# Kernel tuning notes

Measured on AMD Instinct MI355X. Metric: run time of the kernel, lower is better.

## Reference

```python
import jax, jax.numpy as jnp
import numpy as np

E = 8       # num_experts
K = 2       # top_k
N = 16384   # tokens
H = 2048    # hidden_dim
B = 128     # bottleneck_dim
EPS = 1e-6


def setup_inputs() -> dict:
    key = jax.random.key(0)
    ks = jax.random.split(key, 8)
    x = jax.random.normal(ks[0], (N, H), dtype=jnp.float32)
    skin_probs = jax.random.uniform(ks[1], (N, 3), dtype=jnp.float32)
    # routers (torch Linear weight layout: [out, in])
    W_img = jax.random.normal(ks[2], (E, H), dtype=jnp.float32) * 0.02
    W_skin = jax.random.normal(ks[3], (E, 3), dtype=jnp.float32) * 0.02
    # stacked expert params: Linear(H->B) then Linear(B->H)
    W1 = jax.random.normal(ks[4], (E, B, H), dtype=jnp.float32) * 0.02
    b1 = jax.random.normal(ks[5], (E, B), dtype=jnp.float32) * 0.02
    W2 = jax.random.normal(ks[6], (E, H, B), dtype=jnp.float32) * 0.02
    b2 = jax.random.normal(ks[7], (E, H), dtype=jnp.float32) * 0.02
    return {"x": x, "skin_probs": skin_probs, "W_img": W_img, "W_skin": W_skin,
            "W1": W1, "b1": b1, "W2": W2, "b2": b2}


def reference(x, skin_probs, W_img, W_skin, W1, b1, W2, b2):
    # router
    router_logits = x @ W_img.T + skin_probs @ W_skin.T          # [N, E]
    router_probs = jax.nn.softmax(router_logits, axis=-1)        # [N, E]
    top_v, top_i = jax.lax.top_k(router_probs, K)                 # [N, K]
    top_v = top_v / (top_v.sum(axis=-1, keepdims=True) + EPS)
    sel = jax.nn.one_hot(top_i, E, dtype=x.dtype)                 # [N, K, E], 0/1
    w = (sel * top_v[..., None]).sum(axis=1)                      # [N, E] combine weights (0 if not selected)
    # experts, dense-equivalent combine: out = sum_e w[n,e] * (relu(x W1_e^T + b1_e) W2_e^T + b2_e)
    h = jax.nn.relu(jnp.einsum('nh,ebh->neb', x, W1) + b1)        # [N, E, B]
    moe = jnp.einsum('neb,ehb->nh', h * w[:, :, None], W2) + w @ b2  # [N, H]
    out = x + moe
    # aux load-balancing loss
    mean_prob = router_probs.mean(axis=0)                         # [E]
    mean_freq = sel.sum(axis=1).mean(axis=0)                      # [E]
    aux_loss = (mean_prob * mean_freq).sum() * E
    return out, aux_loss
```

## Files before the change

### kernel.cpp

```cpp
#include <hip/hip_runtime.h>

#define N_TOK 16384
#define HD    2048
#define BD    128
#define NE    8
#define KEXT  1088

typedef float  f32x4  __attribute__((ext_vector_type(4)));
typedef __bf16 bf16x8 __attribute__((ext_vector_type(8)));
typedef unsigned short u16;
typedef unsigned short u16x4 __attribute__((ext_vector_type(4)));

__device__ __forceinline__ u16 f2bf(float f) {
  union { float f; unsigned u; } v; v.f = f;
  unsigned u = v.u;
  return (u16)((u + 0x7FFFu + ((u >> 16) & 1u)) >> 16);
}

__device__ __forceinline__ void gload16(const void* g, void* l) {
  __builtin_amdgcn_global_load_lds(
      (const __attribute__((address_space(1))) void*)g,
      (__attribute__((address_space(3))) void*)l, 16, 0, 0);
}

__global__ void init_aux_k(float* p) {
  if (threadIdx.x < 16) p[threadIdx.x] = 0.f;
}

__global__ __launch_bounds__(256) void conv_w1_k(const float* __restrict__ W1,
                                                 u16* __restrict__ W1b) {
  int i = (blockIdx.x * 256 + threadIdx.x) * 4;
  float4 v = *(const float4*)(W1 + i);
  u16x4 o; o.x = f2bf(v.x); o.y = f2bf(v.y); o.z = f2bf(v.z); o.w = f2bf(v.w);
  *(u16x4*)(W1b + i) = o;
}

__global__ __launch_bounds__(256) void conv_w2_k(const float* __restrict__ W2,
                                                 const float* __restrict__ b2,
                                                 u16* __restrict__ Bt2) {
  int i4 = (blockIdx.x * 256 + threadIdx.x) * 4;
  int h = i4 / KEXT, j0 = i4 % KEXT;
  u16x4 o;
  #pragma unroll
  for (int c = 0; c < 4; c++) {
    int j = j0 + c;
    float v;
    if (j < 1024) {
      int e = j >> 7, b = j & 127;
      v = W2[((size_t)e * HD + h) * BD + b];
    } else if (j < 1032) {
      v = b2[(size_t)(j - 1024) * HD + h];
    } else {
      v = 0.f;
    }
    if (c == 0) o.x = f2bf(v); else if (c == 1) o.y = f2bf(v);
    else if (c == 2) o.z = f2bf(v); else o.w = f2bf(v);
  }
  *(u16x4*)(Bt2 + i4) = o;
}

__global__ __launch_bounds__(256)
void router_k(const float* __restrict__ x, const float* __restrict__ skin,
              const float* __restrict__ Wimg, const float* __restrict__ Wskin,
              u16* __restrict__ xbf, float* __restrict__ wout,
              u16* __restrict__ h2, float* __restrict__ psum,
              float* __restrict__ cnt) {
  __shared__ float red[16];
  int t = threadIdx.x;
  int l = t & 63, wv = t >> 6;
  float pacc = 0.f, cacc = 0.f;

  for (int it = 0; it < 4; it++) {
    int n = blockIdx.x * 16 + wv * 4 + it;
    const float4* xr = (const float4*)(x + (size_t)n * HD);
    u16* xo = xbf + (size_t)n * HD;
    float4 xv[8];
    #pragma unroll
    for (int j = 0; j < 8; j++) {
      xv[j] = xr[j * 64 + l];
      u16x4 o; o.x = f2bf(xv[j].x); o.y = f2bf(xv[j].y);
      o.z = f2bf(xv[j].z); o.w = f2bf(xv[j].w);
      *(u16x4*)(xo + j * 256 + l * 4) = o;
    }
    float acc[NE];
    #pragma unroll
    for (int e = 0; e < NE; e++) {
      const float4* wr = (const float4*)(Wimg + (size_t)e * HD);
      float a = 0.f;
      #pragma unroll
      for (int j = 0; j < 8; j++) {
        float4 w4 = wr[j * 64 + l];
        a += xv[j].x * w4.x + xv[j].y * w4.y + xv[j].z * w4.z + xv[j].w * w4.w;
      }
      acc[e] = a;
    }
    float logit[NE];
    #pragma unroll
    for (int e = 0; e < NE; e++) {
      float v = acc[e];
      for (int off = 32; off >= 1; off >>= 1) v += __shfl_xor(v, off);
      logit[e] = v + skin[n * 3 + 0] * Wskin[e * 3 + 0]
                   + skin[n * 3 + 1] * Wskin[e * 3 + 1]
                   + skin[n * 3 + 2] * Wskin[e * 3 + 2];
    }
    float mx = logit[0];
    #pragma unroll
    for (int e = 1; e < NE; e++) mx = fmaxf(mx, logit[e]);
    float p[NE], s = 0.f;
    #pragma unroll
    for (int e = 0; e < NE; e++) { p[e] = expf(logit[e] - mx); s += p[e]; }
    float inv = 1.f / s;
    #pragma unroll
    for (int e = 0; e < NE; e++) p[e] *= inv;
    int i1 = 0; float v1 = p[0];
    #pragma unroll
    for (int e = 1; e < NE; e++) if (p[e] > v1) { v1 = p[e]; i1 = e; }
    int i2 = -1; float v2 = -1.f;
    #pragma unroll
    for (int e = 0; e < NE; e++) if (e != i1 && p[e] > v2) { v2 = p[e]; i2 = e; }
    float denom = v1 + v2 + 1e-6f;
    float w1v = v1 / denom, w2v = v2 / denom;
    float wl = (l == i1) ? w1v : ((l == i2) ? w2v : 0.f);
    if (l < NE) wout[(size_t)n * NE + l] = wl;
    h2[(size_t)n * KEXT + 1024 + l] = (l < NE) ? f2bf(wl) : (u16)0;
    if (l < NE) { pacc += p[l]; cacc += (l == i1 ? 1.f : 0.f) + (l == i2 ? 1.f : 0.f); }
  }
  __syncthreads();
  if (t < 16) red[t] = 0.f;
  __syncthreads();
  if (l < NE) { atomicAdd(&red[l], pacc); atomicAdd(&red[NE + l], cacc); }
  __syncthreads();
  if (t < 8)       atomicAdd(&psum[t], red[t]);
  else if (t < 16) atomicAdd(&cnt[t - 8], red[t]);
}

template <int EPI>
__global__ __launch_bounds__(256)
void gemm_bt(const u16* __restrict__ A, int lda,
             const u16* __restrict__ Bt, int ldb,
             int K, int NB, int chunk,
             const float* __restrict__ b1, const float* __restrict__ w,
             u16* __restrict__ Hout,
             const float* __restrict__ xres, float* __restrict__ out) {
  __shared__ u16 lA[128 * 64];
  __shared__ u16 lB[128 * 64];
  int xcd = blockIdx.x & 7, idxw = blockIdx.x >> 3;
  int lin = xcd * chunk + idxw;
  int bn = lin % NB, bm = lin / NB;

  int t = threadIdx.x;
  int l = t & 63, wv = t >> 6;
  int wr = wv >> 1, wc = wv & 1;
  int r = t >> 3;
  int cl = (t & 7) * 8;
  int cs = (((t & 7) ^ (r & 7))) * 8;

  const u16* Ag = A + (size_t)(bm * 128 + r) * lda + cs;
  const u16* Bg = Bt + (size_t)(bn * 128 + r) * ldb + cs;
  u16* lAp = &lA[r * 64 + cl];
  u16* lBp = &lB[r * 64 + cl];

  int swz = (l & 7) << 4;

  f32x4 acc[4][4];
  #pragma unroll
  for (int m = 0; m < 4; m++)
    #pragma unroll
    for (int n = 0; n < 4; n++) acc[m][n] = (f32x4){0.f, 0.f, 0.f, 0.f};

  for (int k0 = 0; k0 < K; k0 += 64) {
    #pragma unroll
    for (int i = 0; i < 4; i++) {
      gload16(Ag + (size_t)i * 32 * lda + k0, lAp + i * 32 * 64);
      gload16(Bg + (size_t)i * 32 * ldb + k0, lBp + i * 32 * 64);
    }
    __syncthreads();
    #pragma unroll
    for (int kk = 0; kk < 64; kk += 32) {
      int cb = (kk + (l >> 4) * 8) * 2;
      int co = cb ^ swz;
      bf16x8 a[4], b[4];
      #pragma unroll
      for (int m = 0; m < 4; m++) {
        int Ra = wr * 64 + m * 16 + (l & 15);
        a[m] = *(const bf16x8*)((const char*)lA + Ra * 128 + co);
      }
      #pragma unroll
      for (int n = 0; n < 4; n++) {
        int Rb = wc * 64 + n * 16 + (l & 15);
        b[n] = *(const bf16x8*)((const char*)lB + Rb * 128 + co);
      }
      #pragma unroll
      for (int m = 0; m < 4; m++)
        #pragma unroll
        for (int n = 0; n < 4; n++)
          acc[m][n] = __builtin_amdgcn_mfma_f32_16x16x32_bf16(a[m], b[n], acc[m][n], 0, 0, 0);
    }
    __syncthreads();
  }

  int row0 = bm * 128 + wr * 64 + (l >> 4) * 4;
  int col0 = bn * 128 + wc * 64 + (l & 15);
  if (EPI == 1) {
    #pragma unroll
    for (int n = 0; n < 4; n++) {
      int col = col0 + n * 16;
      float b1v = b1[col];
      #pragma unroll
      for (int m = 0; m < 4; m++) {
        #pragma unroll
        for (int j = 0; j < 4; j++) {
          int row = row0 + m * 16 + j;
          float v = acc[m][n][j] + b1v;
          v = v > 0.f ? v : 0.f;
          v *= w[(size_t)row * NE + bn];
          Hout[(size_t)row * KEXT + col] = f2bf(v);
        }
      }
    }
  } else {
    #pragma unroll
    for (int m = 0; m < 4; m++) {
      #pragma unroll
      for (int j = 0; j < 4; j++) {
        int row = row0 + m * 16 + j;
        const float* xr = xres + (size_t)row * HD;
        float* orow = out + (size_t)row * HD;
        #pragma unroll
        for (int n = 0; n < 4; n++) {
          int col = col0 + n * 16;
          orow[col] = acc[m][n][j] + xr[col];
        }
      }
    }
  }
}

__global__ void aux_fin_k(const float* __restrict__ psum,
                          const float* __restrict__ cnt,
                          float* __restrict__ out) {
  if (threadIdx.x == 0) {
    float a = 0.f;
    for (int e = 0; e < NE; e++)
      a += (psum[e] / (float)N_TOK) * (cnt[e] / (float)N_TOK);
    out[(size_t)N_TOK * HD] = a * (float)NE;
  }
}

extern "C" void kernel_launch(void* const* d_in, const int* in_sizes, int n_in,
                              void* d_out, int out_size, void* d_ws, size_t ws_size,
                              hipStream_t stream) {
  const float* x     = (const float*)d_in[0];
  const float* skin  = (const float*)d_in[1];
  const float* Wimg  = (const float*)d_in[2];
  const float* Wskin = (const float*)d_in[3];
  const float* W1    = (const float*)d_in[4];
  const float* b1    = (const float*)d_in[5];
  const float* W2    = (const float*)d_in[6];
  const float* b2    = (const float*)d_in[7];
  float* out = (float*)d_out;

  char* ws = (char*)d_ws;
  u16*   xbf  = (u16*)(ws);
  float* wout = (float*)(ws + 67108864);
  u16*   h2   = (u16*)(ws + 67633152);
  u16*   W1b  = (u16*)(ws + 103284736);
  u16*   Bt2  = (u16*)(ws + 107479040);
  float* aux  = (float*)(ws + 111935488);
  float* psum = aux;
  float* cnt  = aux + 8;

  init_aux_k<<<1, 64, 0, stream>>>(aux);
  conv_w1_k<<<(NE * BD * HD) / (256 * 4), 256, 0, stream>>>(W1, W1b);
  conv_w2_k<<<(HD * KEXT) / (256 * 4), 256, 0, stream>>>(W2, b2, Bt2);
  router_k<<<N_TOK / 16, 256, 0, stream>>>(x, skin, Wimg, Wskin, xbf, wout, h2,
                                           psum, cnt);
  aux_fin_k<<<1, 64, 0, stream>>>(psum, cnt, out);
  gemm_bt<1><<<(N_TOK / 128) * (1024 / 128), 256, 0, stream>>>(
      xbf, HD, W1b, HD, HD, 1024 / 128, ((N_TOK / 128) * (1024 / 128)) / 8,
      b1, wout, h2, nullptr, nullptr);
  gemm_bt<2><<<(N_TOK / 128) * (HD / 128), 256, 0, stream>>>(
      h2, KEXT, Bt2, KEXT, KEXT, HD / 128, ((N_TOK / 128) * (HD / 128)) / 8,
      nullptr, nullptr, nullptr, x, out);
}
```

Before: 510.0 us.

## Replace 128x128 GEMM with double-buffered 256x256 tile kernel using 8 waves

```diff
diff --git a/kernel.cpp b/kernel.cpp
--- a/kernel.cpp
+++ b/kernel.cpp
@@ -135,100 +135,165 @@
 }
 
 template <int EPI>
-__global__ __launch_bounds__(256)
-void gemm_bt(const u16* __restrict__ A, int lda,
+__global__ __launch_bounds__(512, 2)
+void gemm256(const u16* __restrict__ A, int lda,
              const u16* __restrict__ Bt, int ldb,
              int K, int NB, int chunk,
              const float* __restrict__ b1, const float* __restrict__ w,
              u16* __restrict__ Hout,
              const float* __restrict__ xres, float* __restrict__ out) {
-  __shared__ u16 lA[128 * 64];
-  __shared__ u16 lB[128 * 64];
+  __shared__ u16 sm[2][2][256 * 64];
+
+  const int t = threadIdx.x;
+  const int l = t & 63, wv = t >> 6;
+  const int wm = wv >> 2, wn = wv & 3;
+  const int r = t >> 3;
+  const int cdst = (t & 7) * 8;
+  const int csrc = ((t & 7) ^ (r & 7)) * 8;
+
   int xcd = blockIdx.x & 7, idxw = blockIdx.x >> 3;
   int lin = xcd * chunk + idxw;
   int bn = lin % NB, bm = lin / NB;
 
-  int t = threadIdx.x;
-  int l = t & 63, wv = t >> 6;
-  int wr = wv >> 1, wc = wv & 1;
-  int r = t >> 3;
-  int cl = (t & 7) * 8;
-  int cs = (((t & 7) ^ (r & 7))) * 8;
-
-  const u16* Ag = A + (size_t)(bm * 128 + r) * lda + cs;
-  const u16* Bg = Bt + (size_t)(bn * 128 + r) * ldb + cs;
-  u16* lAp = &lA[r * 64 + cl];
-  u16* lBp = &lB[r * 64 + cl];
-
-  int swz = (l & 7) << 4;
-
-  f32x4 acc[4][4];
+  const u16* Ag = A + (size_t)(bm * 256 + r) * lda + csrc;
+  const u16* Bg = Bt + (size_t)(bn * 256 + r) * ldb + csrc;
+
+  auto stage = [&](int buf, int i, int k0) {
+    gload16(Ag + (size_t)i * 64 * lda + k0, &sm[buf][0][(i * 64 + r) * 64 + cdst]);
+    gload16(Bg + (size_t)i * 64 * ldb + k0, &sm[buf][1][(i * 64 + r) * 64 + cdst]);
+  };
+  auto rdfrag = [&](const u16* base, int row, int kbyte) -> bf16x8 {
+    int byte = (row * 128 + kbyte + (l >> 4) * 16) ^ ((row & 7) << 4);
+    return *(const bf16x8*)((const char*)base + byte);
+  };
+
+  f32x4 acc[8][4];
   #pragma unroll
-  for (int m = 0; m < 4; m++)
+  for (int m = 0; m < 8; m++)
     #pragma unroll
     for (int n = 0; n < 4; n++) acc[m][n] = (f32x4){0.f, 0.f, 0.f, 0.f};
 
+  bf16x8 afr[4][2];
+  bf16x8 bfr[4][2];
+
+  #pragma unroll
+  for (int i = 0; i < 4; i++) stage(0, i, 0);
+  asm volatile("s_waitcnt vmcnt(0)" ::: "memory");
+  __builtin_amdgcn_s_barrier();
+  __builtin_amdgcn_sched_barrier(0);
+
+  int cur = 0;
   for (int k0 = 0; k0 < K; k0 += 64) {
-    #pragma unroll
-    for (int i = 0; i < 4; i++) {
-      gload16(Ag + (size_t)i * 32 * lda + k0, lAp + i * 32 * 64);
-      gload16(Bg + (size_t)i * 32 * ldb + k0, lBp + i * 32 * 64);
-    }
-    __syncthreads();
-    #pragma unroll
-    for (int kk = 0; kk < 64; kk += 32) {
-      int cb = (kk + (l >> 4) * 8) * 2;
-      int co = cb ^ swz;
-      bf16x8 a[4], b[4];
-      #pragma unroll
-      for (int m = 0; m < 4; m++) {
-        int Ra = wr * 64 + m * 16 + (l & 15);
-        a[m] = *(const bf16x8*)((const char*)lA + Ra * 128 + co);
-      }
-      #pragma unroll
-      for (int n = 0; n < 4; n++) {
-        int Rb = wc * 64 + n * 16 + (l & 15);
-        b[n] = *(const bf16x8*)((const char*)lB + Rb * 128 + co);
-      }
-      #pragma unroll
-      for (int m = 0; m < 4; m++)
-        #pragma unroll
-        for (int n = 0; n < 4; n++)
-          acc[m][n] = __builtin_amdgcn_mfma_f32_16x16x32_bf16(a[m], b[n], acc[m][n], 0, 0, 0);
-    }
-    __syncthreads();
-  }
-
-  int row0 = bm * 128 + wr * 64 + (l >> 4) * 4;
-  int col0 = bn * 128 + wc * 64 + (l & 15);
+    const u16* cA = sm[cur][0];
+    const u16* cB = sm[cur][1];
+    const int nxt = cur ^ 1, kn = k0 + 64;
+    const bool pf = kn < K;
+
+    #pragma unroll
+    for (int mi = 0; mi < 4; mi++) {
+      int row = wm * 128 + mi * 16 + (l & 15);
+      afr[mi][0] = rdfrag(cA, row, 0); afr[mi][1] = rdfrag(cA, row, 64);
+    }
+    #pragma unroll
+    for (int n = 0; n < 2; n++) {
+      int row = wn * 64 + n * 16 + (l & 15);
+      bfr[n][0] = rdfrag(cB, row, 0); bfr[n][1] = rdfrag(cB, row, 64);
+    }
+    if (pf) stage(nxt, 0, kn);
+    __builtin_amdgcn_s_barrier();
+    __builtin_amdgcn_s_setprio(1);
+    #pragma unroll
+    for (int mi = 0; mi < 4; mi++)
+      #pragma unroll
+      for (int n = 0; n < 2; n++) {
+        acc[mi][n] = __builtin_amdgcn_mfma_f32_16x16x32_bf16(afr[mi][0], bfr[n][0], acc[mi][n], 0, 0, 0);
+        acc[mi][n] = __builtin_amdgcn_mfma_f32_16x16x32_bf16(afr[mi][1], bfr[n][1], acc[mi][n], 0, 0, 0);
+      }
+    __builtin_amdgcn_s_setprio(0);
+    __builtin_amdgcn_s_barrier();
+
+    #pragma unroll
+    for (int n = 2; n < 4; n++) {
+      int row = wn * 64 + n * 16 + (l & 15);
+      bfr[n][0] = rdfrag(cB, row, 0); bfr[n][1] = rdfrag(cB, row, 64);
+    }
+    if (pf) stage(nxt, 1, kn);
+    __builtin_amdgcn_s_barrier();
+    __builtin_amdgcn_s_setprio(1);
+    #pragma unroll
+    for (int mi = 0; mi < 4; mi++)
+      #pragma unroll
+      for (int n = 2; n < 4; n++) {
+        acc[mi][n] = __builtin_amdgcn_mfma_f32_16x16x32_bf16(afr[mi][0], bfr[n][0], acc[mi][n], 0, 0, 0);
+        acc[mi][n] = __builtin_amdgcn_mfma_f32_16x16x32_bf16(afr[mi][1], bfr[n][1], acc[mi][n], 0, 0, 0);
+      }
+    __builtin_amdgcn_s_setprio(0);
+    __builtin_amdgcn_s_barrier();
+
+    #pragma unroll
+    for (int mi = 0; mi < 4; mi++) {
+      int row = wm * 128 + 64 + mi * 16 + (l & 15);
+      afr[mi][0] = rdfrag(cA, row, 0); afr[mi][1] = rdfrag(cA, row, 64);
+    }
+    if (pf) stage(nxt, 2, kn);
+    __builtin_amdgcn_s_barrier();
+    __builtin_amdgcn_s_setprio(1);
+    #pragma unroll
+    for (int mi = 0; mi < 4; mi++)
+      #pragma unroll
+      for (int n = 0; n < 2; n++) {
+        acc[4 + mi][n] = __builtin_amdgcn_mfma_f32_16x16x32_bf16(afr[mi][0], bfr[n][0], acc[4 + mi][n], 0, 0, 0);
+        acc[4 + mi][n] = __builtin_amdgcn_mfma_f32_16x16x32_bf16(afr[mi][1], bfr[n][1], acc[4 + mi][n], 0, 0, 0);
+      }
+    __builtin_amdgcn_s_setprio(0);
+    __builtin_amdgcn_s_barrier();
+
+    if (pf) stage(nxt, 3, kn);
+    __builtin_amdgcn_s_barrier();
+    __builtin_amdgcn_s_setprio(1);
+    #pragma unroll
+    for (int mi = 0; mi < 4; mi++)
+      #pragma unroll
+      for (int n = 2; n < 4; n++) {
+        acc[4 + mi][n] = __builtin_amdgcn_mfma_f32_16x16x32_bf16(afr[mi][0], bfr[n][0], acc[4 + mi][n], 0, 0, 0);
+        acc[4 + mi][n] = __builtin_amdgcn_mfma_f32_16x16x32_bf16(afr[mi][1], bfr[n][1], acc[4 + mi][n], 0, 0, 0);
+      }
+    __builtin_amdgcn_s_setprio(0);
+
+    asm volatile("s_waitcnt vmcnt(0)" ::: "memory");
+    __builtin_amdgcn_s_barrier();
+    __builtin_amdgcn_sched_barrier(0);
+    cur = nxt;
+  }
+
   if (EPI == 1) {
+    int ew = bn * 2 + (wn >> 1);
     #pragma unroll
     for (int n = 0; n < 4; n++) {
-      int col = col0 + n * 16;
+      int col = bn * 256 + wn * 64 + n * 16 + (l & 15);
       float b1v = b1[col];
       #pragma unroll
-      for (int m = 0; m < 4; m++) {
+      for (int m = 0; m < 8; m++) {
         #pragma unroll
         for (int j = 0; j < 4; j++) {
-          int row = row0 + m * 16 + j;
+          int row = bm * 256 + wm * 128 + m * 16 + (l >> 4) * 4 + j;
           float v = acc[m][n][j] + b1v;
-          v = v > 0.f ? v : 0.f;
-          v *= w[(size_t)row * NE + bn];
+          v = fmaxf(v, 0.f) * w[(size_t)row * NE + ew];
           Hout[(size_t)row * KEXT + col] = f2bf(v);
         }
       }
     }
   } else {
     #pragma unroll
-    for (int m = 0; m < 4; m++) {
+    for (int m = 0; m < 8; m++) {
       #pragma unroll
       for (int j = 0; j < 4; j++) {
-        int row = row0 + m * 16 + j;
+        int row = bm * 256 + wm * 128 + m * 16 + (l >> 4) * 4 + j;
         const float* xr = xres + (size_t)row * HD;
         float* orow = out + (size_t)row * HD;
         #pragma unroll
         for (int n = 0; n < 4; n++) {
-          int col = col0 + n * 16;
+          int col = bn * 256 + wn * 64 + n * 16 + (l & 15);
           orow[col] = acc[m][n][j] + xr[col];
         }
       }
@@ -276,10 +341,10 @@
   router_k<<<N_TOK / 16, 256, 0, stream>>>(x, skin, Wimg, Wskin, xbf, wout, h2,
                                            psum, cnt);
   aux_fin_k<<<1, 64, 0, stream>>>(psum, cnt, out);
-  gemm_bt<1><<<(N_TOK / 128) * (1024 / 128), 256, 0, stream>>>(
-      xbf, HD, W1b, HD, HD, 1024 / 128, ((N_TOK / 128) * (1024 / 128)) / 8,
+  gemm256<1><<<(N_TOK / 256) * (1024 / 256), 512, 0, stream>>>(
+      xbf, HD, W1b, HD, HD, 1024 / 256, ((N_TOK / 256) * (1024 / 256)) / 8,
       b1, wout, h2, nullptr, nullptr);
-  gemm_bt<2><<<(N_TOK / 128) * (HD / 128), 256, 0, stream>>>(
-      h2, KEXT, Bt2, KEXT, KEXT, HD / 128, ((N_TOK / 128) * (HD / 128)) / 8,
+  gemm256<2><<<(N_TOK / 256) * (HD / 256), 512, 0, stream>>>(
+      h2, KEXT, Bt2, KEXT, KEXT, HD / 256, ((N_TOK / 256) * (HD / 256)) / 8,
       nullptr, nullptr, nullptr, x, out);
 }
```

After: 498.6 us. -2.2%, faster.
